# Kernel tuning notes

Hardware: AMD Instinct MI355X
Metric: run time of the kernel (lower is better)

## Reference

```python
import jax, jax.numpy as jnp
import numpy as np

B, T, E = 2, 2048, 1024   # batch, block_size, emb_d
H, D = 16, 64             # heads, head_size


def setup_inputs() -> dict:
    key = jax.random.key(0)
    ks = jax.random.split(key, 7)
    s = 1.0 / np.sqrt(E)
    inputs = jax.random.normal(ks[0], (B, T, E), dtype=jnp.float32)
    k_w = jax.random.uniform(ks[1], (H, E, D), jnp.float32, -s, s)
    k_b = jax.random.uniform(ks[2], (H, D), jnp.float32, -s, s)
    q_w = jax.random.uniform(ks[3], (H, E, D), jnp.float32, -s, s)
    q_b = jax.random.uniform(ks[4], (H, D), jnp.float32, -s, s)
    v_w = jax.random.uniform(ks[5], (H, E, D), jnp.float32, -s, s)
    v_b = jax.random.uniform(ks[6], (H, D), jnp.float32, -s, s)
    return {"inputs": inputs, "k_w": k_w, "k_b": k_b,
            "q_w": q_w, "q_b": q_b, "v_w": v_w, "v_b": v_b}


def reference(inputs, k_w, k_b, q_w, q_b, v_w, v_b):
    # Per-head linear projections, vectorized over heads: (B,T,E)x(H,E,D)->(B,H,T,D)
    k = jnp.einsum('bte,hed->bhtd', inputs, k_w) + k_b[None, :, None, :]
    q = jnp.einsum('bte,hed->bhtd', inputs, q_w) + q_b[None, :, None, :]
    v = jnp.einsum('bte,hed->bhtd', inputs, v_w) + v_b[None, :, None, :]

    scale = D ** (-0.5)
    # scores: (B,H,Tq,Tk)
    w = jnp.einsum('bhtd,bhsd->bhts', q, k) * scale
    tril = jnp.tril(jnp.ones((T, T), dtype=bool))
    w = jnp.where(tril[None, None, :, :], w, -jnp.inf)
    # NOTE: original torch code does softmax(weights, dim=1) on a (B,T,T)
    # tensor, i.e. over the QUERY axis. Faithfully reproduce: axis=-2 here.
    w = jax.nn.softmax(w, axis=-2)
    out = jnp.einsum('bhts,bhsd->bhtd', w, v)           # (B,H,T,D)
    # concat heads along last dim, head-major order matching torch.cat
    return out.transpose(0, 2, 1, 3).reshape(B, T, H * D)
```

## Files before the change

kernel.cpp:

```cpp
#include <hip/hip_runtime.h>
#include <hip/hip_bf16.h>
#include <math.h>

#define B_ 2
#define T_ 2048
#define E_ 1024
#define H_ 16
#define D_ 64
#define NT_ 32
#define QSCALE 0.180336880f

typedef __attribute__((ext_vector_type(8))) short bf16x8;
typedef __attribute__((ext_vector_type(4))) float f32x4;

#if __has_builtin(__builtin_amdgcn_exp2f)
#define EXP2(x) __builtin_amdgcn_exp2f(x)
#else
#define EXP2(x) exp2f(x)
#endif

__device__ __forceinline__ unsigned short f2bf(float x) {
  union { float f; unsigned u; } v; v.f = x;
  unsigned r = v.u + 0x7FFFu + ((v.u >> 16) & 1u);
  return (unsigned short)(r >> 16);
}
__device__ __forceinline__ unsigned pk2bf(float a, float b) {
  __hip_bfloat162 h = __float22bfloat162_rn(make_float2(a, b));
  union { __hip_bfloat162 h; unsigned u; } c; c.h = h; return c.u;
}

__device__ __forceinline__ void dma8(const unsigned short* g, int gstride,
                                     unsigned short* l, int lane)
{
  const int r = lane >> 3, bg = (lane & 7) ^ (r & 7);
  __builtin_amdgcn_global_load_lds(
      (const __attribute__((address_space(1))) void*)(g + (size_t)r * gstride + bg * 8),
      (__attribute__((address_space(3))) void*)l, 16, 0, 0);
}
__device__ __forceinline__ bf16x8 frag(const unsigned short* tile, int row, int g) {
  return *(const bf16x8*)(tile + row * 64 + (((g ^ row) & 7) << 3));
}

__global__ __launch_bounds__(256) void pack_kernel(
    const float* __restrict__ in, unsigned short* __restrict__ o16,
    const float* __restrict__ qw, const float* __restrict__ kw, const float* __restrict__ vw,
    unsigned short* __restrict__ qwt, unsigned short* __restrict__ kwt,
    unsigned short* __restrict__ vwt)
{
  __shared__ float s[64][65];
  const int tid = threadIdx.x;
  if (blockIdx.x < 2048) {
    const size_t i = ((size_t)blockIdx.x * 256 + tid) * 8;
    float4 f0 = *(const float4*)(in + i);
    float4 f1 = *(const float4*)(in + i + 4);
    unsigned u[4] = { pk2bf(f0.x, f0.y), pk2bf(f0.z, f0.w),
                      pk2bf(f1.x, f1.y), pk2bf(f1.z, f1.w) };
    *(bf16x8*)(o16 + i) = *(const bf16x8*)u;
    return;
  }
  const int i = blockIdx.x - 2048;
  const int e0 = (i & 15) * 64, h = (i >> 4) & 15, z = i >> 8;
  const float* w = (z == 0) ? qw : (z == 1) ? kw : vw;
  unsigned short* o = (z == 0) ? qwt : (z == 1) ? kwt : vwt;
  {
    const int r = tid >> 2;
    #pragma unroll
    for (int p = 0; p < 4; ++p) {
      const int c = (tid & 3) * 4 + p * 16;
      float4 f = *(const float4*)(w + ((size_t)(h * E_ + e0 + r)) * D_ + c);
      s[r][c] = f.x; s[r][c+1] = f.y; s[r][c+2] = f.z; s[r][c+3] = f.w;
    }
  }
  __syncthreads();
  {
    const int d = tid >> 2, ec = (tid & 3) * 16;
    unsigned short tmp[16];
    #pragma unroll
    for (int j = 0; j < 16; ++j) tmp[j] = f2bf(s[ec + j][d]);
    unsigned short* dst = o + ((size_t)(h * D_ + d)) * E_ + e0 + ec;
    *(bf16x8*)(dst)     = *(const bf16x8*)&tmp[0];
    *(bf16x8*)(dst + 8) = *(const bf16x8*)&tmp[8];
  }
}

__global__ __launch_bounds__(256) void proj_kernel(
    const unsigned short* __restrict__ in16,
    const unsigned short* __restrict__ qwt, const unsigned short* __restrict__ kwt,
    const unsigned short* __restrict__ vwt,
    const float* __restrict__ qb, const float* __restrict__ kb, const float* __restrict__ vb,
    unsigned short* __restrict__ qo, unsigned short* __restrict__ ko,
    unsigned short* __restrict__ vt)
{
  __shared__ __align__(16) unsigned short in_s[2][128 * 64];
  __shared__ __align__(16) unsigned short w_s[2][3 * 64 * 64];
  const int tid = threadIdx.x;
  const int lane = tid & 63, wv = tid >> 6;
  const int l15 = lane & 15, quad = lane >> 4;
  const int t0 = blockIdx.x * 128, h = blockIdx.y, b = blockIdx.z;
  const int bh = b * H_ + h;
  const unsigned short* wts[3] = { qwt, kwt, vwt };

  f32x4 acc[3][8];
  #pragma unroll
  for (int x = 0; x < 3; ++x)
    #pragma unroll
    for (int tb = 0; tb < 8; ++tb) acc[x][tb] = (f32x4){0.f, 0.f, 0.f, 0.f};

#define PROJ_STAGE(e0_, bi_)                                                      \
  {                                                                               \
    const unsigned short* gin = in16 + ((size_t)(b * T_ + t0)) * E_ + (e0_);      \
    _Pragma("unroll")                                                             \
    for (int p = 0; p < 4; ++p) {                                                 \
      const int br = wv * 32 + p * 8;                                             \
      dma8(gin + (size_t)br * E_, E_, &in_s[bi_][br * 64], lane);                 \
    }                                                                             \
    _Pragma("unroll")                                                             \
    for (int j = 0; j < 6; ++j) {                                                 \
      const int idx = wv * 6 + j;                                                 \
      const int x = idx >> 3, br = (idx & 7) * 8;                                 \
      dma8(wts[x] + ((size_t)(h * D_ + br)) * E_ + (e0_), E_,                     \
           &w_s[bi_][x * 4096 + br * 64], lane);                                  \
    }                                                                             \
  }

  PROJ_STAGE(0, 0);
  __syncthreads();
  for (int e = 0; e < 16; ++e) {
    const int bi = e & 1;
    if (e < 15) PROJ_STAGE((e + 1) * 64, bi ^ 1);
    const unsigned short* is = in_s[bi];
    const unsigned short* ws = w_s[bi];
    #pragma unroll
    for (int kk = 0; kk < 2; ++kk) {
      const int g0 = kk * 4 + quad;
      bf16x8 bfr[3];
      #pragma unroll
      for (int x = 0; x < 3; ++x)
        bfr[x] = frag(ws, x * 64 + wv * 16 + l15, g0);
      bf16x8 afr[8];
      #pragma unroll
      for (int tb = 0; tb < 8; ++tb)
        afr[tb] = frag(is, tb * 16 + l15, g0);
      #pragma unroll
      for (int tb = 0; tb < 8; ++tb) {
        acc[0][tb] = __builtin_amdgcn_mfma_f32_16x16x32_bf16(bfr[0], afr[tb], acc[0][tb], 0, 0, 0);
        acc[1][tb] = __builtin_amdgcn_mfma_f32_16x16x32_bf16(bfr[1], afr[tb], acc[1][tb], 0, 0, 0);
        acc[2][tb] = __builtin_amdgcn_mfma_f32_16x16x32_bf16(afr[tb], bfr[2], acc[2][tb], 0, 0, 0);
      }
    }
    __syncthreads();
  }
#undef PROJ_STAGE

  const size_t obase = (size_t)bh * T_;
  #pragma unroll
  for (int x = 0; x < 2; ++x) {
    const float scl = (x == 0) ? QSCALE : 1.0f;
    const float* bias = (x == 0) ? qb : kb;
    unsigned short* outp = (x == 0) ? qo : ko;
    float bias4[4];
    *(float4*)bias4 = *(const float4*)&bias[h * D_ + wv * 16 + quad * 4];
    #pragma unroll
    for (int tb = 0; tb < 8; ++tb) {
      const int t = t0 + tb * 16 + l15;
      unsigned short pk[4];
      #pragma unroll
      for (int r = 0; r < 4; ++r) pk[r] = f2bf((acc[x][tb][r] + bias4[r]) * scl);
      *(ushort4*)(outp + (obase + t) * D_ + wv * 16 + quad * 4) = *(const ushort4*)pk;
    }
  }
  {
    const int d = wv * 16 + l15;
    const float bvv = vb[h * D_ + d];
    #pragma unroll
    for (int tb = 0; tb < 8; ++tb) {
      const int t = t0 + tb * 16 + quad * 4;
      unsigned short pk[4];
      #pragma unroll
      for (int r = 0; r < 4; ++r) pk[r] = f2bf(acc[2][tb][r] + bvv);
      *(ushort4*)(vt + ((size_t)(bh * D_ + d)) * T_ + t) = *(const ushort4*)pk;
    }
  }
}

__global__ __launch_bounds__(256) void stats_kernel(
    const unsigned short* __restrict__ q, const unsigned short* __restrict__ k,
    float* __restrict__ lg)
{
  __shared__ __align__(16) unsigned short q_s[2][64 * 64];
  __shared__ float red[4][64];
  const int tid = threadIdx.x;
  const int lane = tid & 63, wv = tid >> 6;
  const int l15 = lane & 15, quad = lane >> 4;
  const int h = blockIdx.x, b = blockIdx.y, sa = blockIdx.z;
  const int bh = b * H_ + h;
  const int s0 = sa * 64;
  const unsigned short* qbase = q + (size_t)bh * T_ * 64;

  bf16x8 kf[4][2];
  #pragma unroll
  for (int nb = 0; nb < 4; ++nb)
    #pragma unroll
    for (int kk = 0; kk < 2; ++kk)
      kf[nb][kk] = *(const bf16x8*)(k + ((size_t)(bh * T_ + s0 + nb * 16 + l15)) * 64
                                      + kk * 32 + quad * 8);

  #pragma unroll
  for (int pp = 0; pp < 2; ++pp) {
    const int br = wv * 16 + pp * 8;
    dma8(qbase + (size_t)(sa * 64 + br) * 64, 64, &q_s[0][br * 64], lane);
  }
  __syncthreads();

  float lsum[4] = {0.f, 0.f, 0.f, 0.f};

  for (int tt = sa, i = 0; tt < NT_; ++tt, ++i) {
    const int bi = i & 1;
    if (tt + 1 < NT_) {
      #pragma unroll
      for (int pp = 0; pp < 2; ++pp) {
        const int br = wv * 16 + pp * 8;
        dma8(qbase + (size_t)((tt + 1) * 64 + br) * 64, 64, &q_s[bi ^ 1][br * 64], lane);
      }
    }
    bf16x8 a0 = frag(q_s[bi], wv * 16 + l15, quad);
    bf16x8 a1 = frag(q_s[bi], wv * 16 + l15, 4 + quad);
    f32x4 sacc[4];
    #pragma unroll
    for (int nb = 0; nb < 4; ++nb) sacc[nb] = (f32x4){0.f, 0.f, 0.f, 0.f};
    #pragma unroll
    for (int nb = 0; nb < 4; ++nb) {
      sacc[nb] = __builtin_amdgcn_mfma_f32_16x16x32_bf16(a0, kf[nb][0], sacc[nb], 0, 0, 0);
      sacc[nb] = __builtin_amdgcn_mfma_f32_16x16x32_bf16(a1, kf[nb][1], sacc[nb], 0, 0, 0);
    }
    if (tt == sa) {
      const int tbase = tt * 64 + wv * 16 + quad * 4;
      #pragma unroll
      for (int nb = 0; nb < 4; ++nb) {
        const int s = s0 + nb * 16 + l15;
        #pragma unroll
        for (int r = 0; r < 4; ++r)
          lsum[nb] += (tbase + r >= s) ? EXP2(sacc[nb][r]) : 0.f;
      }
    } else {
      #pragma unroll
      for (int nb = 0; nb < 4; ++nb)
        #pragma unroll
        for (int r = 0; r < 4; ++r) lsum[nb] += EXP2(sacc[nb][r]);
    }
    __syncthreads();
  }
  #pragma unroll
  for (int nb = 0; nb < 4; ++nb) {
    lsum[nb] += __shfl_xor(lsum[nb], 16);
    lsum[nb] += __shfl_xor(lsum[nb], 32);
  }
  if (lane < 16) {
    #pragma unroll
    for (int nb = 0; nb < 4; ++nb) red[wv][nb * 16 + lane] = lsum[nb];
  }
  __syncthreads();
  if (tid < 64) {
    const float L = red[0][tid] + red[1][tid] + red[2][tid] + red[3][tid];
    lg[(size_t)bh * T_ + s0 + tid] = -__log2f(L);
  }
}

__global__ __launch_bounds__(256) void out_kernel(
    const unsigned short* __restrict__ q, const unsigned short* __restrict__ k,
    const unsigned short* __restrict__ vt, const float* __restrict__ lg,
    float* __restrict__ out)
{
  __shared__ __align__(16) unsigned short k_s[2][64 * 64];
  __shared__ __align__(16) unsigned short vt_s[2][64 * 64];
  __shared__ __align__(16) unsigned short u_s[4][16][72];
  __shared__ float lg_sh[2][64];
  const int tid = threadIdx.x;
  const int lane = tid & 63, wv = tid >> 6;
  const int l15 = lane & 15, quad = lane >> 4;
  const int h = blockIdx.x, b = blockIdx.y, jt = 31 - blockIdx.z;
  const int bh = b * H_ + h;
  const int t0 = jt * 64;
  const unsigned short* kbase = k + (size_t)bh * T_ * 64;
  const unsigned short* vbase = vt + (size_t)bh * D_ * T_;
  const float* lgbase = lg + (size_t)bh * T_;

  const unsigned short* qrow = q + (size_t)(bh * T_ + t0 + wv * 16 + l15) * 64;
  bf16x8 qf0 = *(const bf16x8*)(qrow + quad * 8);
  bf16x8 qf1 = *(const bf16x8*)(qrow + 32 + quad * 8);

  #pragma unroll
  for (int pp = 0; pp < 2; ++pp) {
    const int br = wv * 16 + pp * 8;
    dma8(kbase + (size_t)br * 64, 64, &k_s[0][br * 64], lane);
    dma8(vbase + (size_t)br * T_, T_, &vt_s[0][br * 64], lane);
  }
  if (tid < 64) lg_sh[0][tid] = lgbase[tid];
  __syncthreads();

  f32x4 oacc[4];
  #pragma unroll
  for (int nb = 0; nb < 4; ++nb) oacc[nb] = (f32x4){0.f, 0.f, 0.f, 0.f};

  unsigned short* urow = &u_s[wv][l15][0];
  const int tcol = t0 + wv * 16 + l15;

  for (int st = 0; st <= jt; ++st) {
    const int bi = st & 1;
    if (st < jt) {
      const int s1 = (st + 1) * 64;
      #pragma unroll
      for (int pp = 0; pp < 2; ++pp) {
        const int br = wv * 16 + pp * 8;
        dma8(kbase + (size_t)(s1 + br) * 64, 64, &k_s[bi ^ 1][br * 64], lane);
        dma8(vbase + (size_t)br * T_ + s1, T_, &vt_s[bi ^ 1][br * 64], lane);
      }
      if (tid < 64) lg_sh[bi ^ 1][tid] = lgbase[s1 + tid];
    }
    const int s0 = st * 64;
    const unsigned short* ks = k_s[bi];
    const unsigned short* vs = vt_s[bi];
    const float* lgb = lg_sh[bi];
    f32x4 sacc[4];
    #pragma unroll
    for (int mb = 0; mb < 4; ++mb) {
      float lg4[4];
      *(float4*)lg4 = *(const float4*)&lgb[mb * 16 + quad * 4];
      sacc[mb] = (f32x4){lg4[0], lg4[1], lg4[2], lg4[3]};
    }
    #pragma unroll
    for (int mb = 0; mb < 4; ++mb) {
      bf16x8 ka0 = frag(ks, mb * 16 + l15, quad);
      bf16x8 ka1 = frag(ks, mb * 16 + l15, 4 + quad);
      sacc[mb] = __builtin_amdgcn_mfma_f32_16x16x32_bf16(ka0, qf0, sacc[mb], 0, 0, 0);
      sacc[mb] = __builtin_amdgcn_mfma_f32_16x16x32_bf16(ka1, qf1, sacc[mb], 0, 0, 0);
    }
    if (st == jt) {
      #pragma unroll
      for (int mb = 0; mb < 4; ++mb) {
        const int sbase = s0 + mb * 16 + quad * 4;
        float uu[4] = { EXP2(sacc[mb][0]), EXP2(sacc[mb][1]),
                        EXP2(sacc[mb][2]), EXP2(sacc[mb][3]) };
        #pragma unroll
        for (int r = 0; r < 4; ++r) if (tcol < sbase + r) uu[r] = 0.f;
        *(uint2*)(urow + mb * 16 + quad * 4) =
            make_uint2(pk2bf(uu[0], uu[1]), pk2bf(uu[2], uu[3]));
      }
    } else {
      #pragma unroll
      for (int mb = 0; mb < 4; ++mb) {
        float uu[4] = { EXP2(sacc[mb][0]), EXP2(sacc[mb][1]),
                        EXP2(sacc[mb][2]), EXP2(sacc[mb][3]) };
        *(uint2*)(urow + mb * 16 + quad * 4) =
            make_uint2(pk2bf(uu[0], uu[1]), pk2bf(uu[2], uu[3]));
      }
    }
    #pragma unroll
    for (int kk = 0; kk < 2; ++kk) {
      bf16x8 ua = *(const bf16x8*)(urow + kk * 32 + quad * 8);
      #pragma unroll
      for (int nb = 0; nb < 4; ++nb)
        oacc[nb] = __builtin_amdgcn_mfma_f32_16x16x32_bf16(
            frag(vs, nb * 16 + l15, kk * 4 + quad), ua, oacc[nb], 0, 0, 0);
    }
    __syncthreads();
  }
  float* orow = out + ((size_t)(b * T_ + t0 + wv * 16 + l15)) * (H_ * D_) + h * D_;
  #pragma unroll
  for (int nb = 0; nb < 4; ++nb) {
    float o4[4] = { oacc[nb][0], oacc[nb][1], oacc[nb][2], oacc[nb][3] };
    *(float4*)(orow + nb * 16 + quad * 4) = *(const float4*)o4;
  }
}

extern "C" void kernel_launch(void* const* d_in, const int* in_sizes, int n_in,
                              void* d_out, int out_size, void* d_ws, size_t ws_size,
                              hipStream_t stream) {
  const float* in = (const float*)d_in[0];
  const float* kw = (const float*)d_in[1];
  const float* kb = (const float*)d_in[2];
  const float* qw = (const float*)d_in[3];
  const float* qb = (const float*)d_in[4];
  const float* vw = (const float*)d_in[5];
  const float* vb = (const float*)d_in[6];
  float* out = (float*)d_out;

  unsigned short* p = (unsigned short*)d_ws;
  const size_t inz = (size_t)B_ * T_ * E_;
  const size_t wz  = (size_t)H_ * D_ * E_;
  const size_t qz  = (size_t)B_ * H_ * T_ * D_;
  unsigned short* in16 = p;            p += inz;
  unsigned short* qwt  = p;            p += wz;
  unsigned short* kwt  = p;            p += wz;
  unsigned short* vwt  = p;            p += wz;
  unsigned short* q16  = p;            p += qz;
  unsigned short* k16  = p;            p += qz;
  unsigned short* vtb  = p;            p += qz;
  float* lgbuf = (float*)p;

  dim3 blk(256);
  pack_kernel <<<dim3(2048 + 768), blk, 0, stream>>>(in, in16, qw, kw, vw, qwt, kwt, vwt);
  proj_kernel <<<dim3(T_ / 128, H_, B_), blk, 0, stream>>>(in16, qwt, kwt, vwt,
                                                           qb, kb, vb, q16, k16, vtb);
  stats_kernel<<<dim3(H_, B_, NT_), blk, 0, stream>>>(q16, k16, lgbuf);
  out_kernel  <<<dim3(H_, B_, NT_), blk, 0, stream>>>(q16, k16, vtb, lgbuf, out);
}
```

Baseline: 170.9 us.

## Fold softmax normalizer into V and load Q fragments directly from global

The stats kernel now computes the reciprocal of each key's column sum and scales the corresponding transposed V entries in place, instead of writing a log2 normalizer that out_kernel added into every score accumulator. out_kernel starts its score accumulators at zero and no longer loads the per-tile normalizer. The stats kernel also drops its LDS double-buffer and per-iteration barrier, prefetching Q fragments straight into registers from global memory. The in-place V rescale adds an extra bf16 rounding step on V and makes the V buffer depend on the stats pass.

```diff
diff --git a/kernel.cpp b/kernel.cpp
--- a/kernel.cpp
+++ b/kernel.cpp
@@ -23,6 +23,9 @@
   union { float f; unsigned u; } v; v.f = x;
   unsigned r = v.u + 0x7FFFu + ((v.u >> 16) & 1u);
   return (unsigned short)(r >> 16);
+}
+__device__ __forceinline__ float bf2f(unsigned short u) {
+  union { float f; unsigned u; } v; v.u = ((unsigned)u) << 16; return v.f;
 }
 __device__ __forceinline__ unsigned pk2bf(float a, float b) {
   __hip_bfloat162 h = __float22bfloat162_rn(make_float2(a, b));
@@ -185,10 +188,10 @@
 
 __global__ __launch_bounds__(256) void stats_kernel(
     const unsigned short* __restrict__ q, const unsigned short* __restrict__ k,
-    float* __restrict__ lg)
+    unsigned short* __restrict__ vt)
 {
-  __shared__ __align__(16) unsigned short q_s[2][64 * 64];
   __shared__ float red[4][64];
+  __shared__ float rl_sh[64];
   const int tid = threadIdx.x;
   const int lane = tid & 63, wv = tid >> 6;
   const int l15 = lane & 15, quad = lane >> 4;
@@ -205,26 +208,19 @@
       kf[nb][kk] = *(const bf16x8*)(k + ((size_t)(bh * T_ + s0 + nb * 16 + l15)) * 64
                                       + kk * 32 + quad * 8);
 
-  #pragma unroll
-  for (int pp = 0; pp < 2; ++pp) {
-    const int br = wv * 16 + pp * 8;
-    dma8(qbase + (size_t)(sa * 64 + br) * 64, 64, &q_s[0][br * 64], lane);
-  }
-  __syncthreads();
+  const unsigned short* qr0 = qbase + (size_t)(s0 + wv * 16 + l15) * 64;
+  bf16x8 a0 = *(const bf16x8*)(qr0 + quad * 8);
+  bf16x8 a1 = *(const bf16x8*)(qr0 + 32 + quad * 8);
 
   float lsum[4] = {0.f, 0.f, 0.f, 0.f};
 
-  for (int tt = sa, i = 0; tt < NT_; ++tt, ++i) {
-    const int bi = i & 1;
+  for (int tt = sa; tt < NT_; ++tt) {
+    bf16x8 n0, n1;
     if (tt + 1 < NT_) {
-      #pragma unroll
-      for (int pp = 0; pp < 2; ++pp) {
-        const int br = wv * 16 + pp * 8;
-        dma8(qbase + (size_t)((tt + 1) * 64 + br) * 64, 64, &q_s[bi ^ 1][br * 64], lane);
-      }
-    }
-    bf16x8 a0 = frag(q_s[bi], wv * 16 + l15, quad);
-    bf16x8 a1 = frag(q_s[bi], wv * 16 + l15, 4 + quad);
+      const unsigned short* qn = qbase + (size_t)((tt + 1) * 64 + wv * 16 + l15) * 64;
+      n0 = *(const bf16x8*)(qn + quad * 8);
+      n1 = *(const bf16x8*)(qn + 32 + quad * 8);
+    }
     f32x4 sacc[4];
     #pragma unroll
     for (int nb = 0; nb < 4; ++nb) sacc[nb] = (f32x4){0.f, 0.f, 0.f, 0.f};
@@ -248,7 +244,7 @@
         #pragma unroll
         for (int r = 0; r < 4; ++r) lsum[nb] += EXP2(sacc[nb][r]);
     }
-    __syncthreads();
+    a0 = n0; a1 = n1;
   }
   #pragma unroll
   for (int nb = 0; nb < 4; ++nb) {
@@ -260,21 +256,31 @@
     for (int nb = 0; nb < 4; ++nb) red[wv][nb * 16 + lane] = lsum[nb];
   }
   __syncthreads();
-  if (tid < 64) {
-    const float L = red[0][tid] + red[1][tid] + red[2][tid] + red[3][tid];
-    lg[(size_t)bh * T_ + s0 + tid] = -__log2f(L);
+  if (tid < 64)
+    rl_sh[tid] = 1.0f / (red[0][tid] + red[1][tid] + red[2][tid] + red[3][tid]);
+  __syncthreads();
+  {
+    const int d = tid >> 2, tc = (tid & 3) * 16;
+    unsigned short* vp = vt + ((size_t)(bh * D_ + d)) * T_ + s0 + tc;
+    bf16x8 v0 = *(const bf16x8*)vp;
+    bf16x8 v1 = *(const bf16x8*)(vp + 8);
+    unsigned short o0[8], o1[8];
+    #pragma unroll
+    for (int j = 0; j < 8; ++j) o0[j] = f2bf(bf2f((unsigned short)v0[j]) * rl_sh[tc + j]);
+    #pragma unroll
+    for (int j = 0; j < 8; ++j) o1[j] = f2bf(bf2f((unsigned short)v1[j]) * rl_sh[tc + 8 + j]);
+    *(bf16x8*)vp       = *(const bf16x8*)o0;
+    *(bf16x8*)(vp + 8) = *(const bf16x8*)o1;
   }
 }
 
 __global__ __launch_bounds__(256) void out_kernel(
     const unsigned short* __restrict__ q, const unsigned short* __restrict__ k,
-    const unsigned short* __restrict__ vt, const float* __restrict__ lg,
-    float* __restrict__ out)
+    const unsigned short* __restrict__ vt, float* __restrict__ out)
 {
   __shared__ __align__(16) unsigned short k_s[2][64 * 64];
   __shared__ __align__(16) unsigned short vt_s[2][64 * 64];
   __shared__ __align__(16) unsigned short u_s[4][16][72];
-  __shared__ float lg_sh[2][64];
   const int tid = threadIdx.x;
   const int lane = tid & 63, wv = tid >> 6;
   const int l15 = lane & 15, quad = lane >> 4;
@@ -283,7 +289,6 @@
   const int t0 = jt * 64;
   const unsigned short* kbase = k + (size_t)bh * T_ * 64;
   const unsigned short* vbase = vt + (size_t)bh * D_ * T_;
-  const float* lgbase = lg + (size_t)bh * T_;
 
   const unsigned short* qrow = q + (size_t)(bh * T_ + t0 + wv * 16 + l15) * 64;
   bf16x8 qf0 = *(const bf16x8*)(qrow + quad * 8);
@@ -295,7 +300,6 @@
     dma8(kbase + (size_t)br * 64, 64, &k_s[0][br * 64], lane);
     dma8(vbase + (size_t)br * T_, T_, &vt_s[0][br * 64], lane);
   }
-  if (tid < 64) lg_sh[0][tid] = lgbase[tid];
   __syncthreads();
 
   f32x4 oacc[4];
@@ -315,19 +319,13 @@
         dma8(kbase + (size_t)(s1 + br) * 64, 64, &k_s[bi ^ 1][br * 64], lane);
         dma8(vbase + (size_t)br * T_ + s1, T_, &vt_s[bi ^ 1][br * 64], lane);
       }
-      if (tid < 64) lg_sh[bi ^ 1][tid] = lgbase[s1 + tid];
     }
     const int s0 = st * 64;
     const unsigned short* ks = k_s[bi];
     const unsigned short* vs = vt_s[bi];
-    const float* lgb = lg_sh[bi];
     f32x4 sacc[4];
     #pragma unroll
-    for (int mb = 0; mb < 4; ++mb) {
-      float lg4[4];
-      *(float4*)lg4 = *(const float4*)&lgb[mb * 16 + quad * 4];
-      sacc[mb] = (f32x4){lg4[0], lg4[1], lg4[2], lg4[3]};
-    }
+    for (int mb = 0; mb < 4; ++mb) sacc[mb] = (f32x4){0.f, 0.f, 0.f, 0.f};
     #pragma unroll
     for (int mb = 0; mb < 4; ++mb) {
       bf16x8 ka0 = frag(ks, mb * 16 + l15, quad);
@@ -396,12 +394,11 @@
   unsigned short* q16  = p;            p += qz;
   unsigned short* k16  = p;            p += qz;
   unsigned short* vtb  = p;            p += qz;
-  float* lgbuf = (float*)p;
 
   dim3 blk(256);
   pack_kernel <<<dim3(2048 + 768), blk, 0, stream>>>(in, in16, qw, kw, vw, qwt, kwt, vwt);
   proj_kernel <<<dim3(T_ / 128, H_, B_), blk, 0, stream>>>(in16, qwt, kwt, vwt,
                                                            qb, kb, vb, q16, k16, vtb);
-  stats_kernel<<<dim3(H_, B_, NT_), blk, 0, stream>>>(q16, k16, lgbuf);
-  out_kernel  <<<dim3(H_, B_, NT_), blk, 0, stream>>>(q16, k16, vtb, lgbuf, out);
-}
+  stats_kernel<<<dim3(H_, B_, NT_), blk, 0, stream>>>(q16, k16, vtb);
+  out_kernel  <<<dim3(H_, B_, NT_), blk, 0, stream>>>(q16, k16, vtb, out);
+}
```

Result: no change. 173.8 us (+1.7%).
